# Kernel tuning notes

Hardware: AMD Instinct MI355X
Metric: run time of the kernel (lower is better)

Reference implementation:

```python
import jax, jax.numpy as jnp
import numpy as np

B, T, D = 4, 4096, 1024
G = 16  # num_heads
C = D // G  # head dim = 64


def setup_inputs() -> dict:
    key = jax.random.key(0)
    ks = jax.random.split(key, 12)
    std = np.sqrt(2.0 / (D + D))  # xavier_normal for square [D, D] weights
    inp = {
        'q': jax.random.normal(ks[0], (B, T, D), jnp.float32),
        'k': jax.random.normal(ks[1], (B, T, D), jnp.float32),
        'v': jax.random.normal(ks[2], (B, T, D), jnp.float32),
        'mask': jnp.ones((B, T), jnp.int32),
        'Wq': jax.random.normal(ks[3], (D, D), jnp.float32) * std,
        'bq': jnp.zeros((D,), jnp.float32),
        'Wk': jax.random.normal(ks[4], (D, D), jnp.float32) * std,
        'bk': jnp.zeros((D,), jnp.float32),
        'Wv': jax.random.normal(ks[5], (D, D), jnp.float32) * std,
        'bv': jnp.zeros((D,), jnp.float32),
        'Wo': jax.random.normal(ks[6], (D, D), jnp.float32) * std,
        'bo': jnp.zeros((D,), jnp.float32),
    }
    return inp


def _heads(x):
    # b t (g c) -> b g t c
    b, t, d = x.shape
    return x.reshape(b, t, G, C).transpose(0, 2, 1, 3)


def reference(q, k, v, mask, Wq, bq, Wk, bk, Wv, bv, Wo, bo):
    # projections (torch Linear: x @ W.T + b)
    qp = q @ Wq.T + bq
    kp = k @ Wk.T + bk
    vp = v @ Wv.T + bv
    # ELU(x) + 1 feature map
    qf = jax.nn.elu(qp) + 1.0
    kf = jax.nn.elu(kp) + 1.0
    qh = _heads(qf)  # b g t c
    kh = _heads(kf)
    vh = _heads(vp)
    # mask keys: b k -> b 1 1 k broadcast over heads and channel
    kh = jnp.where(mask[:, None, :, None] == 0, 0.0, kh)
    k_sum = kh.sum(axis=2)  # b g c
    k_v = jnp.einsum('bgtk,bgtv->bgkv', kh, vh)  # b g c_k c_v
    q_k_v = jnp.einsum('bgqk,bgkv->bgqv', qh, k_v)
    q_k_sum = jnp.einsum('bgqc,bgc->bgq', qh, k_sum)
    o = q_k_v / q_k_sum[..., None]  # b g t c
    o = o.transpose(0, 2, 1, 3).reshape(B, T, D)  # b t (g c)
    return o @ Wo.T + bo
```

## Files before the change

### kernel.cpp

```cpp
#include <hip/hip_runtime.h>
#include <stdint.h>

#define G_HEADS 16
#define HDIM    64
#define DMODEL  1024
#define TSEQ    4096
#define BATCH   4
#define NROWS   (BATCH*TSEQ)

typedef __bf16 bf16_t;
typedef bf16_t bf16x8 __attribute__((ext_vector_type(8)));
typedef float  f32x4  __attribute__((ext_vector_type(4)));
typedef float  f32x4e __attribute__((ext_vector_type(4)));
typedef unsigned short u16x4 __attribute__((ext_vector_type(4)));

__device__ __forceinline__ unsigned short bf16_rne(float f){
  uint32_t u = __float_as_uint(f);
  u += 0x7fffu + ((u >> 16) & 1u);
  return (unsigned short)(u >> 16);
}
__device__ __forceinline__ float elu1(float x){ return x > 0.f ? x + 1.f : __expf(x); }

#define AS1 __attribute__((address_space(1)))
#define AS3 __attribute__((address_space(3)))
__device__ __forceinline__ void gl_lds16(const void* g, void* l){
  __builtin_amdgcn_global_load_lds((const AS1 void*)g, (AS3 void*)l, 16, 0, 0);
}

__device__ __forceinline__ f32x4 mfma16(bf16x8 a, bf16x8 b, f32x4 c){
  return __builtin_amdgcn_mfma_f32_16x16x32_bf16(a, b, c, 0, 0, 0);
}

struct CvtArgs {
  const float* src[7];
  unsigned short* dst[7];
  int n4[7];
};

__global__ void cvt_bf16(CvtArgs a){
  int j = blockIdx.y;
  const f32x4e* s = (const f32x4e*)a.src[j];
  u16x4* d = (u16x4*)a.dst[j];
  int n4 = a.n4[j];
  for (int i = blockIdx.x*blockDim.x + threadIdx.x; i < n4; i += gridDim.x*blockDim.x){
    f32x4e v = s[i];
    u16x4 o;
    o[0] = bf16_rne(v[0]); o[1] = bf16_rne(v[1]);
    o[2] = bf16_rne(v[2]); o[3] = bf16_rne(v[3]);
    d[i] = o;
  }
}

struct ProjArgs {
  const unsigned short* X[4];
  const unsigned short* Wt[4];
  const float* bias[4];
  const int* mask;
  unsigned short* outB[3];
  float* outF;
  int mode_base;
};

__global__ __launch_bounds__(256) void gemm_bt(ProjArgs args)
{
  int mode = args.mode_base + blockIdx.z;
  const unsigned short* X = args.X[mode];
  const unsigned short* W = args.Wt[mode];
  const float* bias = args.bias[mode];
  int tm = blockIdx.x & 127, tn = blockIdx.x >> 7;
  int row0 = tm * 128, col0 = tn * 128;
  int tid = threadIdx.x, lane = tid & 63, wid = tid >> 6;
  int wm = wid & 1, wn = wid >> 1;
  __shared__ __align__(16) unsigned short Al[128*32];
  __shared__ __align__(16) unsigned short Bl[128*32];
  int sr = tid >> 2, sc = (tid & 3) * 8;
  const unsigned short* ga = X + (size_t)(row0 + sr)*DMODEL + sc;
  const unsigned short* gb = W + (size_t)(col0 + sr)*DMODEL + sc;
  char* lA = (char*)Al + wid*1024;
  char* lB = (char*)Bl + wid*1024;
  f32x4 acc[4][4] = {};
  int fr = lane & 15, fg = lane >> 4;
  for (int kt = 0; kt < DMODEL; kt += 32){
    gl_lds16(ga + kt,               lA);
    gl_lds16(ga + 64*DMODEL + kt,   lA + 4096);
    gl_lds16(gb + kt,               lB);
    gl_lds16(gb + 64*DMODEL + kt,   lB + 4096);
    __syncthreads();
    bf16x8 af[4], bfr[4];
    #pragma unroll
    for (int mi=0; mi<4; mi++) af[mi]  = *(const bf16x8*)&Al[(wm*64 + mi*16 + fr)*32 + fg*8];
    #pragma unroll
    for (int ni=0; ni<4; ni++) bfr[ni] = *(const bf16x8*)&Bl[(wn*64 + ni*16 + fr)*32 + fg*8];
    #pragma unroll
    for (int mi=0; mi<4; mi++)
      #pragma unroll
      for (int ni=0; ni<4; ni++)
        acc[mi][ni] = mfma16(af[mi], bfr[ni], acc[mi][ni]);
    __syncthreads();
  }
  float bb[4];
  #pragma unroll
  for (int ni=0; ni<4; ni++) bb[ni] = bias[col0 + wn*64 + ni*16 + fr];

  if (mode == 3){
    float* O = args.outF;
    #pragma unroll
    for (int mi=0; mi<4; mi++){
      int gr = row0 + wm*64 + mi*16 + fg*4;
      #pragma unroll
      for (int ni=0; ni<4; ni++){
        int gc = col0 + wn*64 + ni*16 + fr;
        #pragma unroll
        for (int rr=0; rr<4; rr++)
          O[(size_t)(gr+rr)*DMODEL + gc] = acc[mi][ni][rr] + bb[ni];
      }
    }
  } else if (mode == 0){
    unsigned short* O = args.outB[0];
    #pragma unroll
    for (int mi=0; mi<4; mi++){
      int gr = row0 + wm*64 + mi*16 + fg*4;
      #pragma unroll
      for (int ni=0; ni<4; ni++){
        int gc = col0 + wn*64 + ni*16 + fr;
        #pragma unroll
        for (int rr=0; rr<4; rr++){
          float v = elu1(acc[mi][ni][rr] + bb[ni]);
          O[(size_t)(gr+rr)*DMODEL + gc] = bf16_rne(v);
        }
      }
    }
  } else {
    unsigned short* O = args.outB[mode];
    #pragma unroll
    for (int mi=0; mi<4; mi++){
      int gr = row0 + wm*64 + mi*16 + fg*4;
      int b_ = gr >> 12, t_ = gr & (TSEQ-1);
      int mk[4];
      #pragma unroll
      for (int rr=0; rr<4; rr++) mk[rr] = (mode==1) ? args.mask[gr+rr] : 1;
      #pragma unroll
      for (int ni=0; ni<4; ni++){
        int gc = col0 + wn*64 + ni*16 + fr;
        u16x4 st;
        #pragma unroll
        for (int rr=0; rr<4; rr++){
          float v = acc[mi][ni][rr] + bb[ni];
          if (mode==1){ v = elu1(v); if (mk[rr] == 0) v = 0.f; }
          st[rr] = bf16_rne(v);
        }
        *(u16x4*)&O[((size_t)((b_<<10) + gc))*TSEQ + t_] = st;
      }
    }
  }
}

__global__ void kv_reduce(const unsigned short* __restrict__ kfT,
                          const unsigned short* __restrict__ vpT,
                          float* __restrict__ kv, float* __restrict__ ksum)
{
  int bg = blockIdx.x;
  int chunk = blockIdx.y;
  int tid = threadIdx.x, lane = tid & 63, wid = tid >> 6;
  int fr = lane & 15, fg = lane >> 4;
  const unsigned short* A  = kfT + (size_t)bg*HDIM*TSEQ;
  const unsigned short* Bv = vpT + (size_t)bg*HDIM*TSEQ;
  int t0 = chunk*1024 + wid*256;
  f32x4 acc[4][4] = {};
  float ksp[4] = {0.f,0.f,0.f,0.f};
  for (int ks = 0; ks < 256; ks += 32){
    int tc = t0 + ks + fg*8;
    bf16x8 af[4], bfr[4];
    #pragma unroll
    for (int mi=0; mi<4; mi++) af[mi]  = *(const bf16x8*)&A[(size_t)(mi*16+fr)*TSEQ + tc];
    #pragma unroll
    for (int ni=0; ni<4; ni++) bfr[ni] = *(const bf16x8*)&Bv[(size_t)(ni*16+fr)*TSEQ + tc];
    #pragma unroll
    for (int mi=0; mi<4; mi++){
      float s = 0.f;
      #pragma unroll
      for (int j=0;j<8;j++) s += (float)af[mi][j];
      ksp[mi] += s;
    }
    #pragma unroll
    for (int mi=0; mi<4; mi++)
      #pragma unroll
      for (int ni=0; ni<4; ni++)
        acc[mi][ni] = mfma16(af[mi], bfr[ni], acc[mi][ni]);
  }
  #pragma unroll
  for (int mi=0; mi<4; mi++){
    float s2 = ksp[mi];
    s2 += __shfl_xor(s2, 16);
    s2 += __shfl_xor(s2, 32);
    if (lane < 16) atomicAdd(&ksum[bg*HDIM + mi*16 + lane], s2);
  }
  __shared__ float red[4][HDIM*HDIM];
  #pragma unroll
  for (int mi=0; mi<4; mi++)
    #pragma unroll
    for (int ni=0; ni<4; ni++)
      #pragma unroll
      for (int rr=0; rr<4; rr++)
        red[wid][(mi*16+fg*4+rr)*HDIM + ni*16+fr] = acc[mi][ni][rr];
  __syncthreads();
  for (int i = tid; i < HDIM*HDIM; i += 256){
    float s = red[0][i] + red[1][i] + red[2][i] + red[3][i];
    atomicAdd(&kv[(size_t)bg*HDIM*HDIM + i], s);
  }
}

__global__ void qkv_div(const unsigned short* __restrict__ qf,
                        const float* __restrict__ kv,
                        const float* __restrict__ ksum,
                        unsigned short* __restrict__ o_)
{
  int bg = blockIdx.x, mt = blockIdx.y;
  int b = bg >> 4, g = bg & 15;
  int tid = threadIdx.x, lane = tid & 63, wid = tid >> 6;
  __shared__ __align__(16) unsigned short kvT[HDIM*HDIM];
  __shared__ float ksl[HDIM];
  __shared__ float den[4][64];
  for (int i = tid; i < HDIM*HDIM; i += 256){
    int ck = i >> 6, cv = i & 63;
    kvT[cv*HDIM + ck] = bf16_rne(kv[(size_t)bg*HDIM*HDIM + i]);
  }
  if (tid < HDIM) ksl[tid] = ksum[bg*HDIM + tid];
  __syncthreads();
  int fr = lane & 15, fg = lane >> 4;
  bf16x8 bfrag[2][4];
  #pragma unroll
  for (int ks2=0; ks2<2; ks2++)
    #pragma unroll
    for (int ni=0; ni<4; ni++)
      bfrag[ks2][ni] = *(const bf16x8*)&kvT[(ni*16+fr)*HDIM + ks2*32 + fg*8];
  int t0 = mt*256 + wid*64;
  const unsigned short* A = qf + ((size_t)b*TSEQ + t0)*DMODEL + g*HDIM;
  f32x4 acc[4][4] = {};
  float dp[4] = {0.f,0.f,0.f,0.f};
  #pragma unroll
  for (int ks2=0; ks2<2; ks2++){
    bf16x8 af[4];
    #pragma unroll
    for (int mi=0; mi<4; mi++) af[mi] = *(const bf16x8*)&A[(size_t)(mi*16+fr)*DMODEL + ks2*32 + fg*8];
    #pragma unroll
    for (int mi=0; mi<4; mi++){
      float s = 0.f;
      #pragma unroll
      for (int j=0;j<8;j++) s += (float)af[mi][j] * ksl[ks2*32 + fg*8 + j];
      dp[mi] += s;
    }
    #pragma unroll
    for (int mi=0; mi<4; mi++)
      #pragma unroll
      for (int ni=0; ni<4; ni++)
        acc[mi][ni] = mfma16(af[mi], bfrag[ks2][ni], acc[mi][ni]);
  }
  #pragma unroll
  for (int mi=0; mi<4; mi++){
    float s2 = dp[mi];
    s2 += __shfl_xor(s2, 16);
    s2 += __shfl_xor(s2, 32);
    if (lane < 16) den[wid][mi*16 + lane] = s2;
  }
  __syncthreads();
  unsigned short* O = o_ + ((size_t)b*TSEQ + t0)*DMODEL + g*HDIM;
  #pragma unroll
  for (int mi=0; mi<4; mi++)
    #pragma unroll
    for (int ni=0; ni<4; ni++)
      #pragma unroll
      for (int rr=0; rr<4; rr++){
        int lr = mi*16 + fg*4 + rr;
        float val = acc[mi][ni][rr] / den[wid][lr];
        O[(size_t)lr*DMODEL + ni*16 + fr] = bf16_rne(val);
      }
}

extern "C" void kernel_launch(void* const* d_in, const int* in_sizes, int n_in,
                              void* d_out, int out_size, void* d_ws, size_t ws_size,
                              hipStream_t stream)
{
  const float* q  = (const float*)d_in[0];
  const float* k  = (const float*)d_in[1];
  const float* v  = (const float*)d_in[2];
  const int* mask = (const int*)d_in[3];
  const float* Wq = (const float*)d_in[4];
  const float* bq = (const float*)d_in[5];
  const float* Wk = (const float*)d_in[6];
  const float* bk = (const float*)d_in[7];
  const float* Wv = (const float*)d_in[8];
  const float* bv = (const float*)d_in[9];
  const float* Wo = (const float*)d_in[10];
  const float* bo = (const float*)d_in[11];
  float* out = (float*)d_out;

  char* w = (char*)d_ws;
  const size_t SZ_X = (size_t)NROWS*DMODEL*2;
  const size_t SZ_W = (size_t)DMODEL*DMODEL*2;
  unsigned short* Xq  = (unsigned short*)(w);
  unsigned short* Xk  = (unsigned short*)(w + 1*SZ_X);
  unsigned short* Xv  = (unsigned short*)(w + 2*SZ_X);
  unsigned short* qf  = (unsigned short*)(w + 3*SZ_X);
  unsigned short* kfT = (unsigned short*)(w + 4*SZ_X);
  unsigned short* vpT = (unsigned short*)(w + 5*SZ_X);
  unsigned short* o_  = Xq;
  unsigned short* Wqb = (unsigned short*)(w + 6*SZ_X);
  unsigned short* Wkb = (unsigned short*)(w + 6*SZ_X + 1*SZ_W);
  unsigned short* Wvb = (unsigned short*)(w + 6*SZ_X + 2*SZ_W);
  unsigned short* Wob = (unsigned short*)(w + 6*SZ_X + 3*SZ_W);
  float* kv   = (float*)(w + 6*SZ_X + 4*SZ_W);
  float* ksum = (float*)(w + 6*SZ_X + 4*SZ_W + (size_t)64*HDIM*HDIM*4);

  hipMemsetAsync(kv, 0, (size_t)64*HDIM*HDIM*4 + 64*HDIM*4, stream);

  CvtArgs ca;
  ca.src[0]=q;  ca.dst[0]=Xq;  ca.n4[0]=NROWS*DMODEL/4;
  ca.src[1]=k;  ca.dst[1]=Xk;  ca.n4[1]=NROWS*DMODEL/4;
  ca.src[2]=v;  ca.dst[2]=Xv;  ca.n4[2]=NROWS*DMODEL/4;
  ca.src[3]=Wq; ca.dst[3]=Wqb; ca.n4[3]=DMODEL*DMODEL/4;
  ca.src[4]=Wk; ca.dst[4]=Wkb; ca.n4[4]=DMODEL*DMODEL/4;
  ca.src[5]=Wv; ca.dst[5]=Wvb; ca.n4[5]=DMODEL*DMODEL/4;
  ca.src[6]=Wo; ca.dst[6]=Wob; ca.n4[6]=DMODEL*DMODEL/4;
  cvt_bf16<<<dim3(4096,7), 256, 0, stream>>>(ca);

  ProjArgs pa;
  pa.X[0]=Xq;  pa.X[1]=Xk;  pa.X[2]=Xv;  pa.X[3]=o_;
  pa.Wt[0]=Wqb; pa.Wt[1]=Wkb; pa.Wt[2]=Wvb; pa.Wt[3]=Wob;
  pa.bias[0]=bq; pa.bias[1]=bk; pa.bias[2]=bv; pa.bias[3]=bo;
  pa.mask = mask;
  pa.outB[0]=qf; pa.outB[1]=kfT; pa.outB[2]=vpT;
  pa.outF = out;
  pa.mode_base = 0;
  gemm_bt<<<dim3(1024,1,3), 256, 0, stream>>>(pa);

  kv_reduce<<<dim3(64,4), 256, 0, stream>>>(kfT, vpT, kv, ksum);
  qkv_div<<<dim3(64,16), 256, 0, stream>>>(qf, kv, ksum, o_);

  ProjArgs pb = pa;
  pb.mode_base = 3;
  gemm_bt<<<dim3(1024,1,1), 256, 0, stream>>>(pb);
}
```

Baseline: 489.8 us.

## Fuse fp32-to-bf16 input conversion into projection GEMM and drop kv atomics

The projection GEMM now reads the fp32 q/k/v activations directly, converts them to bf16 in registers and stores them to LDS, so the separate conversion pass and its round trip through an intermediate bf16 buffer go away. Only the weights are still pre-converted. kv_reduce is restructured so each block covers the full sequence for half of the value channels and writes its results directly, which removes the atomics and the memset. The costs are that the A-operand load is no longer an async global-to-LDS copy, so latency hiding in the main GEMM may suffer, and kv_reduce runs fewer blocks, each with more serial work.

```diff
diff --git a/kernel.cpp b/kernel.cpp
--- a/kernel.cpp
+++ b/kernel.cpp
@@ -13,12 +13,17 @@
 typedef float  f32x4  __attribute__((ext_vector_type(4)));
 typedef float  f32x4e __attribute__((ext_vector_type(4)));
 typedef unsigned short u16x4 __attribute__((ext_vector_type(4)));
+typedef unsigned short u16x8 __attribute__((ext_vector_type(8)));
 
 __device__ __forceinline__ unsigned short bf16_rne(float f){
   uint32_t u = __float_as_uint(f);
   u += 0x7fffu + ((u >> 16) & 1u);
   return (unsigned short)(u >> 16);
 }
+__device__ __forceinline__ unsigned short bf16_cvt(float f){
+  bf16_t h = (bf16_t)f;
+  return *(unsigned short*)&h;
+}
 __device__ __forceinline__ float elu1(float x){ return x > 0.f ? x + 1.f : __expf(x); }
 
 #define AS1 __attribute__((address_space(1)))
@@ -32,9 +37,9 @@
 }
 
 struct CvtArgs {
-  const float* src[7];
-  unsigned short* dst[7];
-  int n4[7];
+  const float* src[4];
+  unsigned short* dst[4];
+  int n4[4];
 };
 
 __global__ void cvt_bf16(CvtArgs a){
@@ -52,7 +57,8 @@
 }
 
 struct ProjArgs {
-  const unsigned short* X[4];
+  const float* Xf[3];
+  const unsigned short* Xb;
   const unsigned short* Wt[4];
   const float* bias[4];
   const int* mask;
@@ -61,10 +67,10 @@
   int mode_base;
 };
 
+template<int F32A>
 __global__ __launch_bounds__(256) void gemm_bt(ProjArgs args)
 {
   int mode = args.mode_base + blockIdx.z;
-  const unsigned short* X = args.X[mode];
   const unsigned short* W = args.Wt[mode];
   const float* bias = args.bias[mode];
   int tm = blockIdx.x & 127, tn = blockIdx.x >> 7;
@@ -74,30 +80,66 @@
   __shared__ __align__(16) unsigned short Al[128*32];
   __shared__ __align__(16) unsigned short Bl[128*32];
   int sr = tid >> 2, sc = (tid & 3) * 8;
-  const unsigned short* ga = X + (size_t)(row0 + sr)*DMODEL + sc;
   const unsigned short* gb = W + (size_t)(col0 + sr)*DMODEL + sc;
-  char* lA = (char*)Al + wid*1024;
   char* lB = (char*)Bl + wid*1024;
   f32x4 acc[4][4] = {};
   int fr = lane & 15, fg = lane >> 4;
-  for (int kt = 0; kt < DMODEL; kt += 32){
-    gl_lds16(ga + kt,               lA);
-    gl_lds16(ga + 64*DMODEL + kt,   lA + 4096);
-    gl_lds16(gb + kt,               lB);
-    gl_lds16(gb + 64*DMODEL + kt,   lB + 4096);
-    __syncthreads();
-    bf16x8 af[4], bfr[4];
-    #pragma unroll
-    for (int mi=0; mi<4; mi++) af[mi]  = *(const bf16x8*)&Al[(wm*64 + mi*16 + fr)*32 + fg*8];
-    #pragma unroll
-    for (int ni=0; ni<4; ni++) bfr[ni] = *(const bf16x8*)&Bl[(wn*64 + ni*16 + fr)*32 + fg*8];
-    #pragma unroll
-    for (int mi=0; mi<4; mi++)
-      #pragma unroll
-      for (int ni=0; ni<4; ni++)
-        acc[mi][ni] = mfma16(af[mi], bfr[ni], acc[mi][ni]);
-    __syncthreads();
-  }
+
+  if constexpr (F32A){
+    const float* gaf = args.Xf[mode] + (size_t)(row0 + sr)*DMODEL + sc;
+    for (int kt = 0; kt < DMODEL; kt += 32){
+      f32x4 a0 = *(const f32x4*)(gaf + kt);
+      f32x4 a1 = *(const f32x4*)(gaf + kt + 4);
+      f32x4 a2 = *(const f32x4*)(gaf + kt + 64*DMODEL);
+      f32x4 a3 = *(const f32x4*)(gaf + kt + 64*DMODEL + 4);
+      gl_lds16(gb + kt,             lB);
+      gl_lds16(gb + 64*DMODEL + kt, lB + 4096);
+      u16x8 w0, w1;
+      #pragma unroll
+      for (int j=0;j<4;j++){
+        w0[j]   = bf16_cvt(a0[j]);
+        w0[4+j] = bf16_cvt(a1[j]);
+        w1[j]   = bf16_cvt(a2[j]);
+        w1[4+j] = bf16_cvt(a3[j]);
+      }
+      *(u16x8*)&Al[(size_t)sr*32 + (tid&3)*8]      = w0;
+      *(u16x8*)&Al[(size_t)(sr+64)*32 + (tid&3)*8] = w1;
+      __syncthreads();
+      bf16x8 af[4], bfr[4];
+      #pragma unroll
+      for (int mi=0; mi<4; mi++) af[mi]  = *(const bf16x8*)&Al[(wm*64 + mi*16 + fr)*32 + fg*8];
+      #pragma unroll
+      for (int ni=0; ni<4; ni++) bfr[ni] = *(const bf16x8*)&Bl[(wn*64 + ni*16 + fr)*32 + fg*8];
+      #pragma unroll
+      for (int mi=0; mi<4; mi++)
+        #pragma unroll
+        for (int ni=0; ni<4; ni++)
+          acc[mi][ni] = mfma16(af[mi], bfr[ni], acc[mi][ni]);
+      __syncthreads();
+    }
+  } else {
+    const unsigned short* ga = args.Xb + (size_t)(row0 + sr)*DMODEL + sc;
+    char* lA = (char*)Al + wid*1024;
+    for (int kt = 0; kt < DMODEL; kt += 32){
+      gl_lds16(ga + kt,             lA);
+      gl_lds16(ga + 64*DMODEL + kt, lA + 4096);
+      gl_lds16(gb + kt,             lB);
+      gl_lds16(gb + 64*DMODEL + kt, lB + 4096);
+      __syncthreads();
+      bf16x8 af[4], bfr[4];
+      #pragma unroll
+      for (int mi=0; mi<4; mi++) af[mi]  = *(const bf16x8*)&Al[(wm*64 + mi*16 + fr)*32 + fg*8];
+      #pragma unroll
+      for (int ni=0; ni<4; ni++) bfr[ni] = *(const bf16x8*)&Bl[(wn*64 + ni*16 + fr)*32 + fg*8];
+      #pragma unroll
+      for (int mi=0; mi<4; mi++)
+        #pragma unroll
+        for (int ni=0; ni<4; ni++)
+          acc[mi][ni] = mfma16(af[mi], bfr[ni], acc[mi][ni]);
+      __syncthreads();
+    }
+  }
+
   float bb[4];
   #pragma unroll
   for (int ni=0; ni<4; ni++) bb[ni] = bias[col0 + wn*64 + ni*16 + fr];
@@ -155,26 +197,26 @@
   }
 }
 
-__global__ void kv_reduce(const unsigned short* __restrict__ kfT,
+__global__ __launch_bounds__(256) void kv_reduce(const unsigned short* __restrict__ kfT,
                           const unsigned short* __restrict__ vpT,
                           float* __restrict__ kv, float* __restrict__ ksum)
 {
   int bg = blockIdx.x;
-  int chunk = blockIdx.y;
+  int half = blockIdx.y;
   int tid = threadIdx.x, lane = tid & 63, wid = tid >> 6;
   int fr = lane & 15, fg = lane >> 4;
   const unsigned short* A  = kfT + (size_t)bg*HDIM*TSEQ;
-  const unsigned short* Bv = vpT + (size_t)bg*HDIM*TSEQ;
-  int t0 = chunk*1024 + wid*256;
-  f32x4 acc[4][4] = {};
+  const unsigned short* Bv = vpT + (size_t)bg*HDIM*TSEQ + (size_t)half*32*TSEQ;
+  int t0 = wid*1024;
+  f32x4 acc[4][2] = {};
   float ksp[4] = {0.f,0.f,0.f,0.f};
-  for (int ks = 0; ks < 256; ks += 32){
+  for (int ks = 0; ks < 1024; ks += 32){
     int tc = t0 + ks + fg*8;
-    bf16x8 af[4], bfr[4];
+    bf16x8 af[4], bfr[2];
     #pragma unroll
     for (int mi=0; mi<4; mi++) af[mi]  = *(const bf16x8*)&A[(size_t)(mi*16+fr)*TSEQ + tc];
     #pragma unroll
-    for (int ni=0; ni<4; ni++) bfr[ni] = *(const bf16x8*)&Bv[(size_t)(ni*16+fr)*TSEQ + tc];
+    for (int ni=0; ni<2; ni++) bfr[ni] = *(const bf16x8*)&Bv[(size_t)(ni*16+fr)*TSEQ + tc];
     #pragma unroll
     for (int mi=0; mi<4; mi++){
       float s = 0.f;
@@ -185,28 +227,35 @@
     #pragma unroll
     for (int mi=0; mi<4; mi++)
       #pragma unroll
-      for (int ni=0; ni<4; ni++)
+      for (int ni=0; ni<2; ni++)
         acc[mi][ni] = mfma16(af[mi], bfr[ni], acc[mi][ni]);
   }
+  __shared__ float red[4][HDIM][32];
+  __shared__ float redk[4][HDIM];
   #pragma unroll
   for (int mi=0; mi<4; mi++){
     float s2 = ksp[mi];
     s2 += __shfl_xor(s2, 16);
     s2 += __shfl_xor(s2, 32);
-    if (lane < 16) atomicAdd(&ksum[bg*HDIM + mi*16 + lane], s2);
-  }
-  __shared__ float red[4][HDIM*HDIM];
+    if (lane < 16) redk[wid][mi*16 + lane] = s2;
+  }
   #pragma unroll
   for (int mi=0; mi<4; mi++)
     #pragma unroll
-    for (int ni=0; ni<4; ni++)
+    for (int ni=0; ni<2; ni++)
       #pragma unroll
       for (int rr=0; rr<4; rr++)
-        red[wid][(mi*16+fg*4+rr)*HDIM + ni*16+fr] = acc[mi][ni][rr];
+        red[wid][mi*16+fg*4+rr][ni*16+fr] = acc[mi][ni][rr];
   __syncthreads();
-  for (int i = tid; i < HDIM*HDIM; i += 256){
-    float s = red[0][i] + red[1][i] + red[2][i] + red[3][i];
-    atomicAdd(&kv[(size_t)bg*HDIM*HDIM + i], s);
+  float* kvo = kv + (size_t)bg*HDIM*HDIM + half*32;
+  for (int i = tid; i < HDIM*32; i += 256){
+    int ck = i >> 5, cv = i & 31;
+    float s = red[0][ck][cv] + red[1][ck][cv] + red[2][ck][cv] + red[3][ck][cv];
+    kvo[ck*HDIM + cv] = s;
+  }
+  if (half == 0 && tid < HDIM){
+    float s = redk[0][tid] + redk[1][tid] + redk[2][tid] + redk[3][tid];
+    ksum[bg*HDIM + tid] = s;
   }
 }
 
@@ -298,46 +347,39 @@
   char* w = (char*)d_ws;
   const size_t SZ_X = (size_t)NROWS*DMODEL*2;
   const size_t SZ_W = (size_t)DMODEL*DMODEL*2;
-  unsigned short* Xq  = (unsigned short*)(w);
-  unsigned short* Xk  = (unsigned short*)(w + 1*SZ_X);
-  unsigned short* Xv  = (unsigned short*)(w + 2*SZ_X);
-  unsigned short* qf  = (unsigned short*)(w + 3*SZ_X);
-  unsigned short* kfT = (unsigned short*)(w + 4*SZ_X);
-  unsigned short* vpT = (unsigned short*)(w + 5*SZ_X);
-  unsigned short* o_  = Xq;
-  unsigned short* Wqb = (unsigned short*)(w + 6*SZ_X);
-  unsigned short* Wkb = (unsigned short*)(w + 6*SZ_X + 1*SZ_W);
-  unsigned short* Wvb = (unsigned short*)(w + 6*SZ_X + 2*SZ_W);
-  unsigned short* Wob = (unsigned short*)(w + 6*SZ_X + 3*SZ_W);
-  float* kv   = (float*)(w + 6*SZ_X + 4*SZ_W);
-  float* ksum = (float*)(w + 6*SZ_X + 4*SZ_W + (size_t)64*HDIM*HDIM*4);
-
-  hipMemsetAsync(kv, 0, (size_t)64*HDIM*HDIM*4 + 64*HDIM*4, stream);
+  unsigned short* qf  = (unsigned short*)(w);
+  unsigned short* kfT = (unsigned short*)(w + 1*SZ_X);
+  unsigned short* vpT = (unsigned short*)(w + 2*SZ_X);
+  unsigned short* o_  = (unsigned short*)(w + 3*SZ_X);
+  unsigned short* Wqb = (unsigned short*)(w + 4*SZ_X);
+  unsigned short* Wkb = (unsigned short*)(w + 4*SZ_X + 1*SZ_W);
+  unsigned short* Wvb = (unsigned short*)(w + 4*SZ_X + 2*SZ_W);
+  unsigned short* Wob = (unsigned short*)(w + 4*SZ_X + 3*SZ_W);
+  float* kv   = (float*)(w + 4*SZ_X + 4*SZ_W);
+  float* ksum = (float*)(w + 4*SZ_X + 4*SZ_W + (size_t)64*HDIM*HDIM*4);
 
   CvtArgs ca;
-  ca.src[0]=q;  ca.dst[0]=Xq;  ca.n4[0]=NROWS*DMODEL/4;
-  ca.src[1]=k;  ca.dst[1]=Xk;  ca.n4[1]=NROWS*DMODEL/4;
-  ca.src[2]=v;  ca.dst[2]=Xv;  ca.n4[2]=NROWS*DMODEL/4;
-  ca.src[3]=Wq; ca.dst[3]=Wqb; ca.n4[3]=DMODEL*DMODEL/4;
-  ca.src[4]=Wk; ca.dst[4]=Wkb; ca.n4[4]=DMODEL*DMODEL/4;
-  ca.src[5]=Wv; ca.dst[5]=Wvb; ca.n4[5]=DMODEL*DMODEL/4;
-  ca.src[6]=Wo; ca.dst[6]=Wob; ca.n4[6]=DMODEL*DMODEL/4;
-  cvt_bf16<<<dim3(4096,7), 256, 0, stream>>>(ca);
+  ca.src[0]=Wq; ca.dst[0]=Wqb; ca.n4[0]=DMODEL*DMODEL/4;
+  ca.src[1]=Wk; ca.dst[1]=Wkb; ca.n4[1]=DMODEL*DMODEL/4;
+  ca.src[2]=Wv; ca.dst[2]=Wvb; ca.n4[2]=DMODEL*DMODEL/4;
+  ca.src[3]=Wo; ca.dst[3]=Wob; ca.n4[3]=DMODEL*DMODEL/4;
+  cvt_bf16<<<dim3(256,4), 256, 0, stream>>>(ca);
 
   ProjArgs pa;
-  pa.X[0]=Xq;  pa.X[1]=Xk;  pa.X[2]=Xv;  pa.X[3]=o_;
+  pa.Xf[0]=q; pa.Xf[1]=k; pa.Xf[2]=v;
+  pa.Xb = o_;
   pa.Wt[0]=Wqb; pa.Wt[1]=Wkb; pa.Wt[2]=Wvb; pa.Wt[3]=Wob;
   pa.bias[0]=bq; pa.bias[1]=bk; pa.bias[2]=bv; pa.bias[3]=bo;
   pa.mask = mask;
   pa.outB[0]=qf; pa.outB[1]=kfT; pa.outB[2]=vpT;
   pa.outF = out;
   pa.mode_base = 0;
-  gemm_bt<<<dim3(1024,1,3), 256, 0, stream>>>(pa);
-
-  kv_reduce<<<dim3(64,4), 256, 0, stream>>>(kfT, vpT, kv, ksum);
+  gemm_bt<1><<<dim3(1024,1,3), 256, 0, stream>>>(pa);
+
+  kv_reduce<<<dim3(64,2), 256, 0, stream>>>(kfT, vpT, kv, ksum);
   qkv_div<<<dim3(64,16), 256, 0, stream>>>(qf, kv, ksum, o_);
 
   ProjArgs pb = pa;
   pb.mode_base = 3;
-  gemm_bt<<<dim3(1024,1,1), 256, 0, stream>>>(pb);
-}
+  gemm_bt<0><<<dim3(1024,1,1), 256, 0, stream>>>(pb);
+}
```

After: 506.8 us. +3.5%, slower.

## Replace atomic KV reduction with two-stage partial sums and specialize GEMM kernels

Applied to the files above, without the earlier changes.

The KV/ksum reduction now splits the sequence into 8 chunks instead of 4, so 512 blocks run instead of 256. Each block writes its partial sums to scratch space reused from the Xk buffer, and a small second kernel adds them up. This removes the global atomics and the memset. The GEMM is also split into projection and output kernels with the mode known at compile time, which lets the compiler drop the runtime mode branches. The cost is one extra kernel launch plus the extra partial-buffer traffic.

```diff
diff --git a/kernel.cpp b/kernel.cpp
--- a/kernel.cpp
+++ b/kernel.cpp
@@ -61,9 +61,8 @@
   int mode_base;
 };
 
-__global__ __launch_bounds__(256) void gemm_bt(ProjArgs args)
-{
-  int mode = args.mode_base + blockIdx.z;
+__device__ __forceinline__ void gemm_body(const ProjArgs& args, int mode)
+{
   const unsigned short* X = args.X[mode];
   const unsigned short* W = args.Wt[mode];
   const float* bias = args.bias[mode];
@@ -155,9 +154,16 @@
   }
 }
 
-__global__ void kv_reduce(const unsigned short* __restrict__ kfT,
-                          const unsigned short* __restrict__ vpT,
-                          float* __restrict__ kv, float* __restrict__ ksum)
+__global__ __launch_bounds__(256) void gemm_proj(ProjArgs args){
+  gemm_body(args, blockIdx.z);
+}
+__global__ __launch_bounds__(256) void gemm_out(ProjArgs args){
+  gemm_body(args, 3);
+}
+
+__global__ __launch_bounds__(256) void kv_part(const unsigned short* __restrict__ kfT,
+                       const unsigned short* __restrict__ vpT,
+                       float* __restrict__ part_kv, float* __restrict__ part_ksum)
 {
   int bg = blockIdx.x;
   int chunk = blockIdx.y;
@@ -165,10 +171,10 @@
   int fr = lane & 15, fg = lane >> 4;
   const unsigned short* A  = kfT + (size_t)bg*HDIM*TSEQ;
   const unsigned short* Bv = vpT + (size_t)bg*HDIM*TSEQ;
-  int t0 = chunk*1024 + wid*256;
+  int t0 = chunk*512 + wid*128;
   f32x4 acc[4][4] = {};
   float ksp[4] = {0.f,0.f,0.f,0.f};
-  for (int ks = 0; ks < 256; ks += 32){
+  for (int ks = 0; ks < 128; ks += 32){
     int tc = t0 + ks + fg*8;
     bf16x8 af[4], bfr[4];
     #pragma unroll
@@ -193,20 +199,44 @@
     float s2 = ksp[mi];
     s2 += __shfl_xor(s2, 16);
     s2 += __shfl_xor(s2, 32);
-    if (lane < 16) atomicAdd(&ksum[bg*HDIM + mi*16 + lane], s2);
-  }
-  __shared__ float red[4][HDIM*HDIM];
+    if (lane < 16)
+      part_ksum[(((size_t)chunk*64 + bg)*4 + wid)*HDIM + mi*16 + lane] = s2;
+  }
+  __shared__ float red[4][HDIM][HDIM];
   #pragma unroll
   for (int mi=0; mi<4; mi++)
     #pragma unroll
     for (int ni=0; ni<4; ni++)
       #pragma unroll
       for (int rr=0; rr<4; rr++)
-        red[wid][(mi*16+fg*4+rr)*HDIM + ni*16+fr] = acc[mi][ni][rr];
+        red[wid][mi*16+fg*4+rr][ni*16+fr] = acc[mi][ni][rr];
   __syncthreads();
+  float* kvo = part_kv + ((size_t)chunk*64 + bg)*HDIM*HDIM;
   for (int i = tid; i < HDIM*HDIM; i += 256){
-    float s = red[0][i] + red[1][i] + red[2][i] + red[3][i];
-    atomicAdd(&kv[(size_t)bg*HDIM*HDIM + i], s);
+    int ck = i >> 6, cv = i & 63;
+    kvo[i] = red[0][ck][cv] + red[1][ck][cv] + red[2][ck][cv] + red[3][ck][cv];
+  }
+}
+
+__global__ void kv_final(const float* __restrict__ part_kv,
+                         const float* __restrict__ part_ksum,
+                         float* __restrict__ kv, float* __restrict__ ksum)
+{
+  int bg = blockIdx.x, tid = threadIdx.x;
+  for (int i = tid; i < HDIM*HDIM; i += 256){
+    float s = 0.f;
+    #pragma unroll
+    for (int c = 0; c < 8; c++) s += part_kv[((size_t)c*64 + bg)*HDIM*HDIM + i];
+    kv[(size_t)bg*HDIM*HDIM + i] = s;
+  }
+  if (tid < HDIM){
+    float s = 0.f;
+    #pragma unroll
+    for (int c = 0; c < 8; c++)
+      #pragma unroll
+      for (int wdd = 0; wdd < 4; wdd++)
+        s += part_ksum[(((size_t)c*64 + bg)*4 + wdd)*HDIM + tid];
+    ksum[bg*HDIM + tid] = s;
   }
 }
 
@@ -305,14 +335,14 @@
   unsigned short* kfT = (unsigned short*)(w + 4*SZ_X);
   unsigned short* vpT = (unsigned short*)(w + 5*SZ_X);
   unsigned short* o_  = Xq;
+  float* part_kv   = (float*)Xk;
+  float* part_ksum = (float*)(w + 1*SZ_X + (size_t)8*1024*1024);
   unsigned short* Wqb = (unsigned short*)(w + 6*SZ_X);
   unsigned short* Wkb = (unsigned short*)(w + 6*SZ_X + 1*SZ_W);
   unsigned short* Wvb = (unsigned short*)(w + 6*SZ_X + 2*SZ_W);
   unsigned short* Wob = (unsigned short*)(w + 6*SZ_X + 3*SZ_W);
   float* kv   = (float*)(w + 6*SZ_X + 4*SZ_W);
   float* ksum = (float*)(w + 6*SZ_X + 4*SZ_W + (size_t)64*HDIM*HDIM*4);
-
-  hipMemsetAsync(kv, 0, (size_t)64*HDIM*HDIM*4 + 64*HDIM*4, stream);
 
   CvtArgs ca;
   ca.src[0]=q;  ca.dst[0]=Xq;  ca.n4[0]=NROWS*DMODEL/4;
@@ -332,12 +362,11 @@
   pa.outB[0]=qf; pa.outB[1]=kfT; pa.outB[2]=vpT;
   pa.outF = out;
   pa.mode_base = 0;
-  gemm_bt<<<dim3(1024,1,3), 256, 0, stream>>>(pa);
-
-  kv_reduce<<<dim3(64,4), 256, 0, stream>>>(kfT, vpT, kv, ksum);
+  gemm_proj<<<dim3(1024,1,3), 256, 0, stream>>>(pa);
+
+  kv_part<<<dim3(64,8), 256, 0, stream>>>(kfT, vpT, part_kv, part_ksum);
+  kv_final<<<dim3(64), 256, 0, stream>>>(part_kv, part_ksum, kv, ksum);
   qkv_div<<<dim3(64,16), 256, 0, stream>>>(qf, kv, ksum, o_);
 
-  ProjArgs pb = pa;
-  pb.mode_base = 3;
-  gemm_bt<<<dim3(1024,1,1), 256, 0, stream>>>(pb);
-}
+  gemm_out<<<dim3(1024), 256, 0, stream>>>(pa);
+}
```

Result: no change. 490.1 us (+0.1%).
